# Performance work log

Measured on AMD Instinct MI355X. Metric: run time of the kernel, lower is better.

The kernel has to match this reference:

```python
import jax, jax.numpy as jnp
import numpy as np

B, H, S, E = 8, 50, 512, 128
D = 2 * E  # feature dim of inputs


def setup_inputs() -> dict:
    key = jax.random.key(0)
    ks = jax.random.split(key, 10)
    def lin(kw, kb, fan_in, fan_out):
        lim = 1.0 / np.sqrt(fan_in)
        w = jax.random.uniform(kw, (fan_out, fan_in), jnp.float32, -lim, lim)
        b = jax.random.uniform(kb, (fan_out,), jnp.float32, -lim, lim)
        return w, b
    wc_w, wc_b = lin(ks[0], ks[1], D, D)
    wh_w, wh_b = lin(ks[2], ks[3], D, D)
    qt_w, qt_b = lin(ks[4], ks[5], D, 1)
    wf_w, wf_b = lin(ks[6], ks[7], 2 * D, E)
    return {
        "wca_history_embeddings": jax.random.normal(ks[8], (B, H, S, D), jnp.float32),
        "wca_current_embeddings": jax.random.normal(ks[9], (B, S, D), jnp.float32),
        "wc_w": wc_w, "wc_b": wc_b,
        "wh_w": wh_w, "wh_b": wh_b,
        "qt_w": qt_w, "qt_b": qt_b,
        "wf_w": wf_w, "wf_b": wf_b,
    }


def reference(wca_history_embeddings, wca_current_embeddings,
              wc_w, wc_b, wh_w, wh_b, qt_w, qt_b, wf_w, wf_b):
    # history: [B, H, S, D] -> [B, S, H, D]; current: [B, S, D]
    hist = jnp.transpose(wca_history_embeddings, (0, 2, 1, 3))
    wc_out = wca_current_embeddings @ wc_w.T + wc_b          # [B, S, D]
    wh_out = hist @ wh_w.T + wh_b                             # [B, S, H, D]
    combined = jax.nn.sigmoid(wc_out[:, :, None, :] + wh_out) # [B, S, H, D]
    alpha = combined @ qt_w.T + qt_b                          # [B, S, H, 1]
    history_sum = jnp.sum(alpha * hist, axis=2)               # [B, S, D]
    concat = jnp.concatenate([wca_current_embeddings, history_sum], axis=-1)  # [B, S, 2D]
    return concat @ wf_w.T + wf_b                             # [B, S, E]
```

## Files before the change

kernel.cpp:

```cpp
#include <hip/hip_runtime.h>
#include <hip/hip_bf16.h>

#define Hh 50

typedef __attribute__((ext_vector_type(8))) short bf16x8;
typedef __attribute__((ext_vector_type(4))) float f32x4;
typedef __attribute__((ext_vector_type(16))) float f32x16;

static __device__ __forceinline__ short b16(float x) {
    return __builtin_bit_cast(short, __float2bfloat16(x));
}
static __device__ __forceinline__ bf16x8 cvt8(const float* p) {
    f32x4 a = *(const f32x4*)p;
    f32x4 b = *(const f32x4*)(p + 4);
    bf16x8 r;
    r[0] = b16(a[0]); r[1] = b16(a[1]); r[2] = b16(a[2]); r[3] = b16(a[3]);
    r[4] = b16(b[0]); r[5] = b16(b[1]); r[6] = b16(b[2]); r[7] = b16(b[3]);
    return r;
}

__global__ __launch_bounds__(256) void k_prep(const float* __restrict__ w,
                                              short* __restrict__ o) {
    int t = (int)blockIdx.x * 256 + threadIdx.x;
    int p  = t >> 10;
    int ks = (t >> 6) & 15;
    int l  = t & 63;
    int col = p * 32 + (l & 31);
    int k   = ks * 16 + (l >> 5) * 8;
    bf16x8 v = cvt8(w + (size_t)col * 256 + k);
    *(bf16x8*)(o + (size_t)t * 8) = v;
}

__global__ __launch_bounds__(64) void k_wc(const float* __restrict__ cur,
                                           const float* __restrict__ wcw,
                                           const float* __restrict__ wcb,
                                           const float* __restrict__ whb,
                                           float* __restrict__ out) {
    int l = threadIdx.x;
    int m0 = (int)(blockIdx.x >> 2) * 16;
    int ntb = (int)(blockIdx.x & 3) * 4;
    int lk = (l >> 4) * 8;

    bf16x8 Af[8];
#pragma unroll
    for (int k = 0; k < 8; k++)
        Af[k] = cvt8(cur + (size_t)(m0 + (l & 15)) * 256 + k * 32 + lk);

#pragma unroll
    for (int nt = 0; nt < 4; nt++) {
        int col = (ntb + nt) * 16 + (l & 15);
        f32x4 a = {0.f, 0.f, 0.f, 0.f};
#pragma unroll
        for (int k = 0; k < 8; k++) {
            bf16x8 Bf = cvt8(wcw + (size_t)col * 256 + k * 32 + lk);
            a = __builtin_amdgcn_mfma_f32_16x16x32_bf16(Af[k], Bf, a, 0, 0, 0);
        }
        float bias = wcb[col] + whb[col];
        int row = m0 + (l >> 4) * 4;
#pragma unroll
        for (int r = 0; r < 4; r++)
            out[(size_t)(row + r) * 256 + col] = a[r] + bias;
    }
}

__global__ __launch_bounds__(256, 4)
void k_alpha(const float* __restrict__ hist,
             const float* __restrict__ wcplus,
             const short* __restrict__ whpk,
             const float* __restrict__ qtw,
             const float* __restrict__ qtb,
             float* __restrict__ alphaWS) {
    __shared__ __align__(16) char histA[64 * 512];
    __shared__ float alphaP[8][64];

    int tid = threadIdx.x;
    int l = tid & 63;
    int w = tid >> 6;
    int x = (int)blockIdx.x;
    int b = x / 400;
    int rem = x - b * 400;
    int h = rem >> 3;
    int s0 = (rem & 7) * 64;

    const float* hsrc = hist + ((size_t)(b * Hh + h) * 512 + s0) * 256;
#pragma unroll
    for (int i = 0; i < 8; i++) {
        int c = tid + i * 256;
        int r = c >> 5, g = c & 31;
        bf16x8 v = cvt8(hsrc + r * 256 + g * 8);
        *(bf16x8*)(&histA[r * 512 + ((g ^ (r & 15)) << 4)]) = v;
    }
    __syncthreads();

#pragma unroll 1
    for (int pi = 0; pi < 2; pi++) {
        int p = w + pi * 4;
        const short* wqp = whpk + ((size_t)(p * 16) * 64 + l) * 8;
        bf16x8 Af[16];
#pragma unroll
        for (int ks = 0; ks < 16; ks++)
            Af[ks] = *(const bf16x8*)(wqp + ks * 512);

#pragma unroll 1
        for (int nt = 0; nt < 2; nt++) {
            int sl = nt * 32 + (l & 31);
            int s = s0 + sl;

            f32x16 acc;
#pragma unroll
            for (int i = 0; i < 16; i++) acc[i] = 0.f;
#pragma unroll
            for (int ks = 0; ks < 16; ks++) {
                int g = ks * 2 + (l >> 5);
                bf16x8 Bf = *(const bf16x8*)(&histA[sl * 512 + ((g ^ (sl & 15)) << 4)]);
                acc = __builtin_amdgcn_mfma_f32_32x32x16_bf16(Af[ks], Bf, acc, 0, 0, 0);
            }

            const float* wbp = wcplus + (size_t)(b * 512 + s) * 256 + p * 32 + 4 * (l >> 5);
            const float* qp = qtw + p * 32 + 4 * (l >> 5);
            float pal = 0.f;
#pragma unroll
            for (int q = 0; q < 4; q++) {
                f32x4 wq = *(const f32x4*)(wbp + 8 * q);
                f32x4 qv = *(const f32x4*)(qp + 8 * q);
#pragma unroll
                for (int j = 0; j < 4; j++) {
                    float v = acc[q * 4 + j] + wq[j];
                    float sg = __builtin_amdgcn_rcpf(1.0f + __expf(-v));
                    pal += qv[j] * sg;
                }
            }
            pal += __shfl_xor(pal, 32);
            if (l < 32) alphaP[p][sl] = pal;
        }
    }
    __syncthreads();

    if (tid < 64) {
        float a = qtb[0];
#pragma unroll
        for (int p = 0; p < 8; p++) a += alphaP[p][tid];
        alphaWS[(size_t)(b * Hh + h) * 512 + s0 + tid] = a;
    }
}

__global__ __launch_bounds__(256, 8)
void k_hsum(const float* __restrict__ hist,
            const float* __restrict__ alphaWS,
            float* __restrict__ hsum) {
    int tid = threadIdx.x;
    int x = (int)blockIdx.x;
    int b = x >> 7, sc = x & 127;
    int s = sc * 4 + (tid >> 6);
    int d = (tid & 63) * 4;

    const float* hp = hist + ((size_t)(b * Hh) * 512 + s) * 256 + d;
    const float* ap = alphaWS + (size_t)(b * Hh) * 512 + s;
    f32x4 acc = {0.f, 0.f, 0.f, 0.f};
#pragma unroll 2
    for (int h = 0; h < Hh; h++) {
        f32x4 v = *(const f32x4*)(hp + (size_t)h * 512 * 256);
        float a = ap[(size_t)h * 512];
        acc[0] += a * v[0]; acc[1] += a * v[1];
        acc[2] += a * v[2]; acc[3] += a * v[3];
    }
    *(f32x4*)(hsum + ((size_t)b * 512 + s) * 256 + d) = acc;
}

__global__ __launch_bounds__(64) void k_wf(const float* __restrict__ cur,
                                           const float* __restrict__ hsum,
                                           const float* __restrict__ wfw,
                                           const float* __restrict__ wfb,
                                           float* __restrict__ out) {
    int l = threadIdx.x;
    int m0 = (int)(blockIdx.x >> 1) * 16;
    int ntb = (int)(blockIdx.x & 1) * 4;
    int lk = (l >> 4) * 8;

    f32x4 acc[4];
#pragma unroll
    for (int nt = 0; nt < 4; nt++) acc[nt] = (f32x4){0.f, 0.f, 0.f, 0.f};

#pragma unroll
    for (int k = 0; k < 16; k++) {
        int row = m0 + (l & 15);
        bf16x8 Af;
        if (k < 8)
            Af = cvt8(cur + (size_t)row * 256 + k * 32 + lk);
        else
            Af = cvt8(hsum + (size_t)row * 256 + (k - 8) * 32 + lk);
#pragma unroll
        for (int nt = 0; nt < 4; nt++) {
            int col = (ntb + nt) * 16 + (l & 15);
            bf16x8 Bf = cvt8(wfw + (size_t)col * 512 + k * 32 + lk);
            acc[nt] = __builtin_amdgcn_mfma_f32_16x16x32_bf16(Af, Bf, acc[nt], 0, 0, 0);
        }
    }
#pragma unroll
    for (int nt = 0; nt < 4; nt++) {
        int col = (ntb + nt) * 16 + (l & 15);
        float bias = wfb[col];
        int row = m0 + (l >> 4) * 4;
#pragma unroll
        for (int r = 0; r < 4; r++)
            out[(size_t)(row + r) * 128 + col] = acc[nt][r] + bias;
    }
}

extern "C" void kernel_launch(void* const* d_in, const int* in_sizes, int n_in,
                              void* d_out, int out_size, void* d_ws, size_t ws_size,
                              hipStream_t stream) {
    const float* hist = (const float*)d_in[0];
    const float* cur  = (const float*)d_in[1];
    const float* wc_w = (const float*)d_in[2];
    const float* wc_b = (const float*)d_in[3];
    const float* wh_w = (const float*)d_in[4];
    const float* wh_b = (const float*)d_in[5];
    const float* qt_w = (const float*)d_in[6];
    const float* qt_b = (const float*)d_in[7];
    const float* wf_w = (const float*)d_in[8];
    const float* wf_b = (const float*)d_in[9];

    float* wc_ws   = (float*)d_ws;
    float* hsum    = (float*)((char*)d_ws + ((size_t)4 << 20));
    short* whpk    = (short*)((char*)d_ws + ((size_t)8 << 20));
    float* alphaWS = (float*)((char*)d_ws + ((size_t)8 << 20) + 131072);

    k_prep<<<32, 256, 0, stream>>>(wh_w, whpk);
    k_wc<<<1024, 64, 0, stream>>>(cur, wc_w, wc_b, wh_b, wc_ws);
    k_alpha<<<3200, 256, 0, stream>>>(hist, wc_ws, whpk, qt_w, qt_b, alphaWS);
    k_hsum<<<1024, 256, 0, stream>>>(hist, alphaWS, hsum);
    k_wf<<<512, 64, 0, stream>>>(cur, hsum, wf_w, wf_b, (float*)d_out);
}
```

Before: 147.5 us.

## Restructure alpha kernel to 1024-thread blocks with 16x16 MFMA and rework hsum tiling

The alpha kernel now uses 1024-thread blocks covering 128 sequence rows. Each of 16 waves owns one 16-column slice of the Wh weights, keeps it resident in registers, and loops over 8 row subtiles with 16x16x32 MFMAs, reducing per-row partials through lane shuffles. The weight prepack layout changes to match. The hsum kernel stages alpha values in shared memory and has each thread handle 8 features of one sequence position, halving the block count. The goals are to cut weight reloads and the strided global alpha reads, at the cost of more shuffles, a larger shared-memory footprint per block and lower parallelism in hsum.

```diff
diff --git a/kernel.cpp b/kernel.cpp
--- a/kernel.cpp
+++ b/kernel.cpp
@@ -5,7 +5,6 @@
 
 typedef __attribute__((ext_vector_type(8))) short bf16x8;
 typedef __attribute__((ext_vector_type(4))) float f32x4;
-typedef __attribute__((ext_vector_type(16))) float f32x16;
 
 static __device__ __forceinline__ short b16(float x) {
     return __builtin_bit_cast(short, __float2bfloat16(x));
@@ -22,11 +21,11 @@
 __global__ __launch_bounds__(256) void k_prep(const float* __restrict__ w,
                                               short* __restrict__ o) {
     int t = (int)blockIdx.x * 256 + threadIdx.x;
-    int p  = t >> 10;
-    int ks = (t >> 6) & 15;
+    int p  = t >> 9;
+    int ks = (t >> 6) & 7;
     int l  = t & 63;
-    int col = p * 32 + (l & 31);
-    int k   = ks * 16 + (l >> 5) * 8;
+    int col = p * 16 + (l & 15);
+    int k   = ks * 32 + (l >> 4) * 8;
     bf16x8 v = cvt8(w + (size_t)col * 256 + k);
     *(bf16x8*)(o + (size_t)t * 8) = v;
 }
@@ -63,84 +62,73 @@
     }
 }
 
-__global__ __launch_bounds__(256, 4)
+__global__ __launch_bounds__(1024, 4)
 void k_alpha(const float* __restrict__ hist,
              const float* __restrict__ wcplus,
              const short* __restrict__ whpk,
              const float* __restrict__ qtw,
              const float* __restrict__ qtb,
              float* __restrict__ alphaWS) {
-    __shared__ __align__(16) char histA[64 * 512];
-    __shared__ float alphaP[8][64];
+    __shared__ __align__(16) char histA[128 * 512];
+    __shared__ float alphaP[16][128];
 
     int tid = threadIdx.x;
     int l = tid & 63;
     int w = tid >> 6;
-    int x = (int)blockIdx.x;
-    int b = x / 400;
-    int rem = x - b * 400;
-    int h = rem >> 3;
-    int s0 = (rem & 7) * 64;
-
-    const float* hsrc = hist + ((size_t)(b * Hh + h) * 512 + s0) * 256;
-#pragma unroll
-    for (int i = 0; i < 8; i++) {
-        int c = tid + i * 256;
+    int bh = (int)(blockIdx.x >> 2);
+    int s0 = (int)(blockIdx.x & 3) * 128;
+    int b = bh / Hh;
+
+    const float* hsrc = hist + ((size_t)bh * 512 + s0) * 256;
+#pragma unroll
+    for (int i = 0; i < 4; i++) {
+        int c = tid + i * 1024;
         int r = c >> 5, g = c & 31;
-        bf16x8 v = cvt8(hsrc + r * 256 + g * 8);
+        bf16x8 v = cvt8(hsrc + (size_t)c * 8);
         *(bf16x8*)(&histA[r * 512 + ((g ^ (r & 15)) << 4)]) = v;
     }
+
+    bf16x8 Bf[8];
+    const short* wqp = whpk + ((size_t)(w * 8) * 64 + l) * 8;
+#pragma unroll
+    for (int ks = 0; ks < 8; ks++)
+        Bf[ks] = *(const bf16x8*)(wqp + ks * 512);
+
+    int col = w * 16 + (l & 15);
+    float qv = qtw[col];
+    const float* wcp = wcplus + ((size_t)(b * 512 + s0) + (l >> 4) * 4) * 256 + col;
     __syncthreads();
 
 #pragma unroll 1
-    for (int pi = 0; pi < 2; pi++) {
-        int p = w + pi * 4;
-        const short* wqp = whpk + ((size_t)(p * 16) * 64 + l) * 8;
-        bf16x8 Af[16];
-#pragma unroll
-        for (int ks = 0; ks < 16; ks++)
-            Af[ks] = *(const bf16x8*)(wqp + ks * 512);
-
-#pragma unroll 1
-        for (int nt = 0; nt < 2; nt++) {
-            int sl = nt * 32 + (l & 31);
-            int s = s0 + sl;
-
-            f32x16 acc;
-#pragma unroll
-            for (int i = 0; i < 16; i++) acc[i] = 0.f;
-#pragma unroll
-            for (int ks = 0; ks < 16; ks++) {
-                int g = ks * 2 + (l >> 5);
-                bf16x8 Bf = *(const bf16x8*)(&histA[sl * 512 + ((g ^ (sl & 15)) << 4)]);
-                acc = __builtin_amdgcn_mfma_f32_32x32x16_bf16(Af[ks], Bf, acc, 0, 0, 0);
-            }
-
-            const float* wbp = wcplus + (size_t)(b * 512 + s) * 256 + p * 32 + 4 * (l >> 5);
-            const float* qp = qtw + p * 32 + 4 * (l >> 5);
-            float pal = 0.f;
-#pragma unroll
-            for (int q = 0; q < 4; q++) {
-                f32x4 wq = *(const f32x4*)(wbp + 8 * q);
-                f32x4 qv = *(const f32x4*)(qp + 8 * q);
-#pragma unroll
-                for (int j = 0; j < 4; j++) {
-                    float v = acc[q * 4 + j] + wq[j];
-                    float sg = __builtin_amdgcn_rcpf(1.0f + __expf(-v));
-                    pal += qv[j] * sg;
-                }
-            }
-            pal += __shfl_xor(pal, 32);
-            if (l < 32) alphaP[p][sl] = pal;
+    for (int msub = 0; msub < 8; msub++) {
+        int rA = msub * 16 + (l & 15);
+        f32x4 acc = {0.f, 0.f, 0.f, 0.f};
+#pragma unroll
+        for (int ks = 0; ks < 8; ks++) {
+            int g = ks * 4 + (l >> 4);
+            bf16x8 Ah = *(const bf16x8*)(&histA[rA * 512 + ((g ^ (rA & 15)) << 4)]);
+            acc = __builtin_amdgcn_mfma_f32_16x16x32_bf16(Ah, Bf[ks], acc, 0, 0, 0);
+        }
+#pragma unroll
+        for (int r = 0; r < 4; r++) {
+            float bias = wcp[(size_t)(msub * 16 + r) * 256];
+            float v = acc[r] + bias;
+            float pal = qv * __builtin_amdgcn_rcpf(1.0f + __expf(-v));
+            pal += __shfl_xor(pal, 1);
+            pal += __shfl_xor(pal, 2);
+            pal += __shfl_xor(pal, 4);
+            pal += __shfl_xor(pal, 8);
+            if ((l & 15) == 0)
+                alphaP[w][msub * 16 + (l >> 4) * 4 + r] = pal;
         }
     }
     __syncthreads();
 
-    if (tid < 64) {
+    if (tid < 128) {
         float a = qtb[0];
 #pragma unroll
-        for (int p = 0; p < 8; p++) a += alphaP[p][tid];
-        alphaWS[(size_t)(b * Hh + h) * 512 + s0 + tid] = a;
+        for (int p = 0; p < 16; p++) a += alphaP[p][tid];
+        alphaWS[(size_t)blockIdx.x * 128 + tid] = a;
     }
 }
 
@@ -148,23 +136,32 @@
 void k_hsum(const float* __restrict__ hist,
             const float* __restrict__ alphaWS,
             float* __restrict__ hsum) {
+    __shared__ float al[Hh * 8];
     int tid = threadIdx.x;
     int x = (int)blockIdx.x;
-    int b = x >> 7, sc = x & 127;
-    int s = sc * 4 + (tid >> 6);
-    int d = (tid & 63) * 4;
-
-    const float* hp = hist + ((size_t)(b * Hh) * 512 + s) * 256 + d;
-    const float* ap = alphaWS + (size_t)(b * Hh) * 512 + s;
-    f32x4 acc = {0.f, 0.f, 0.f, 0.f};
+    int b = x >> 6, s0 = (x & 63) * 8;
+
+    for (int t = tid; t < Hh * 8; t += 256) {
+        int h = t >> 3, j = t & 7;
+        al[t] = alphaWS[(size_t)(b * Hh + h) * 512 + s0 + j];
+    }
+    __syncthreads();
+
+    int sidx = tid >> 5;
+    int d = (tid & 31) * 8;
+    const float* hp = hist + ((size_t)(b * Hh) * 512 + s0 + sidx) * 256 + d;
+    f32x4 a0 = {0.f, 0.f, 0.f, 0.f}, a1 = {0.f, 0.f, 0.f, 0.f};
 #pragma unroll 2
     for (int h = 0; h < Hh; h++) {
-        f32x4 v = *(const f32x4*)(hp + (size_t)h * 512 * 256);
-        float a = ap[(size_t)h * 512];
-        acc[0] += a * v[0]; acc[1] += a * v[1];
-        acc[2] += a * v[2]; acc[3] += a * v[3];
-    }
-    *(f32x4*)(hsum + ((size_t)b * 512 + s) * 256 + d) = acc;
+        f32x4 v0 = *(const f32x4*)(hp + (size_t)h * 512 * 256);
+        f32x4 v1 = *(const f32x4*)(hp + (size_t)h * 512 * 256 + 4);
+        float a = al[h * 8 + sidx];
+#pragma unroll
+        for (int j = 0; j < 4; j++) { a0[j] += a * v0[j]; a1[j] += a * v1[j]; }
+    }
+    float* op = hsum + ((size_t)b * 512 + s0 + sidx) * 256 + d;
+    *(f32x4*)op = a0;
+    *(f32x4*)(op + 4) = a1;
 }
 
 __global__ __launch_bounds__(64) void k_wf(const float* __restrict__ cur,
@@ -228,7 +225,7 @@
 
     k_prep<<<32, 256, 0, stream>>>(wh_w, whpk);
     k_wc<<<1024, 64, 0, stream>>>(cur, wc_w, wc_b, wh_b, wc_ws);
-    k_alpha<<<3200, 256, 0, stream>>>(hist, wc_ws, whpk, qt_w, qt_b, alphaWS);
-    k_hsum<<<1024, 256, 0, stream>>>(hist, alphaWS, hsum);
+    k_alpha<<<1600, 1024, 0, stream>>>(hist, wc_ws, whpk, qt_w, qt_b, alphaWS);
+    k_hsum<<<512, 256, 0, stream>>>(hist, alphaWS, hsum);
     k_wf<<<512, 64, 0, stream>>>(cur, hsum, wf_w, wf_b, (float*)d_out);
 }
```

After: 205.9 us. 39.6% more time.
